# Performance work log

Hardware: AMD Instinct MI355X
Metric: run time of the kernel (lower is better)

Reference implementation:

```python
import jax, jax.numpy as jnp
import numpy as np

N_WIRES = 10
N_LAYERS = 4


def _cnot(state, c, t):
    # state: (2,)*N_WIRES per-sample state tensor; CNOT(control=c, target=t)
    s0 = jnp.take(state, 0, axis=c)
    s1 = jnp.take(state, 1, axis=c)
    tt = t if t < c else t - 1  # target axis index after removing control axis
    s1 = jnp.flip(s1, axis=tt)  # X on target where control == 1
    return jnp.stack([s0, s1], axis=c)


def _circuit(x, params):
    # x: (N_WIRES,) angles. RY(x_i) on |0> -> [cos(x_i/2), sin(x_i/2)] product state.
    q = jnp.stack([jnp.cos(x / 2), jnp.sin(x / 2)], axis=-1).astype(jnp.complex64)  # (n, 2)
    state = q[0]
    for i in range(1, N_WIRES):
        state = jnp.tensordot(state, q[i], axes=0)  # -> (2,)*N_WIRES
    half = jnp.array([-0.5, 0.5], dtype=jnp.float32)
    for layer in range(N_LAYERS):
        # RZ(params[layer, i]) on each wire: diagonal phase exp(-i*theta/2), exp(+i*theta/2)
        for i in range(N_WIRES):
            ph = jnp.exp(1j * (half * params[layer, i]))  # (2,) complex64
            shape = [1] * N_WIRES
            shape[i] = 2
            state = state * ph.reshape(shape)
        # CNOT ladder 0->1, 1->2, ..., (n-2)->(n-1), then (n-1)->0
        for i in range(N_WIRES - 1):
            state = _cnot(state, i, i + 1)
        state = _cnot(state, N_WIRES - 1, 0)
    return state.reshape(-1)  # (2**N_WIRES,)


def _states(X, params):
    return jax.vmap(lambda x: _circuit(x, params))(X)  # (B, 2**N_WIRES) complex64


def setup_inputs() -> dict:
    key = jax.random.key(0)
    k1, k2, k3 = jax.random.split(key, 3)
    two_pi = 2.0 * np.pi
    X = jax.random.uniform(k1, (4096, N_WIRES), jnp.float32, 0.0, two_pi)
    Y = jax.random.uniform(k2, (4096, N_WIRES), jnp.float32, 0.0, two_pi)
    params = jax.random.normal(k3, (N_LAYERS, N_WIRES), dtype=jnp.float32)
    return {"X": X, "Y": Y, "params": params}


def reference(X, Y, params):
    sX = _states(X, params)                 # (Nx, D) complex64
    sY = _states(Y, params)                 # (Ny, D) complex64
    M = sX @ sY.conj().T                    # (Nx, Ny) complex overlaps
    return M.real ** 2 + M.imag ** 2        # |<psi_x|psi_y>|^2
```

## Files before the change

### kernel.cpp

```cpp
#include <hip/hip_runtime.h>


#define NS 4096
#define NW 10
#define ROWS 32
#define CPT 2

__global__ __launch_bounds__(256) void qkm_fused(
    const float* __restrict__ X, const float* __restrict__ Y,
    float* __restrict__ out) {
    __shared__ float2 xcs[ROWS][NW];

    const int col  = (blockIdx.x * 256 + threadIdx.x) * CPT;
    const int row0 = blockIdx.y * ROWS;

    for (int t = threadIdx.x; t < ROWS * NW; t += 256) {
        int r = t / NW;
        int w = t - r * NW;
        float s, c;
        __sincosf(0.5f * X[(row0 + r) * NW + w], &s, &c);
        xcs[r][w] = make_float2(c, s);
    }

    float yc[NW][CPT], ys[NW][CPT];
#pragma unroll
    for (int j = 0; j < CPT; ++j) {
        const float* yp = Y + (size_t)(col + j) * NW;
#pragma unroll
        for (int w = 0; w < NW; ++w) {
            float s, c;
            __sincosf(0.5f * yp[w], &s, &c);
            yc[w][j] = c;
            ys[w][j] = s;
        }
    }

    __syncthreads();

#pragma unroll 4
    for (int r = 0; r < ROWS; ++r) {
        float p0 = 1.f, p1 = 1.f;
#pragma unroll
        for (int w = 0; w < NW; ++w) {
            const float2 x = xcs[r][w];
            p0 *= fmaf(x.y, ys[w][0], x.x * yc[w][0]);
            p1 *= fmaf(x.y, ys[w][1], x.x * yc[w][1]);
        }
        float2 o;
        o.x = p0 * p0;
        o.y = p1 * p1;
        *reinterpret_cast<float2*>(out + (size_t)(row0 + r) * NS + col) = o;
    }
}

extern "C" void kernel_launch(void* const* d_in, const int* in_sizes, int n_in,
                              void* d_out, int out_size, void* d_ws, size_t ws_size,
                              hipStream_t stream) {
    const float* X = (const float*)d_in[0];
    const float* Y = (const float*)d_in[1];
    float* out = (float*)d_out;

    dim3 grid(NS / (256 * CPT), NS / ROWS);
    qkm_fused<<<grid, 256, 0, stream>>>(X, Y, out);
}
```

Baseline: 89.36 us.

## Factor cos(x) into per-row product and use tan form with packed float2 math

Rewrites each factor cx*cy + sx*sy as cx*(cy + tan(x)*sy). The per-row product of cx is precomputed once per block, which removes one multiply per wire from the inner loop. The inner loop uses ext_vector float2 operations so the compiler can emit packed FMA instructions, and the row data is loaded with 128-bit shared-memory reads. Near-zero cosines are clamped to avoid division by zero, but large tangent values may hurt accuracy. The change also adds an extra block synchronisation.

After: 82.96 us. 1.08x faster.

```diff
diff --git a/kernel.cpp b/kernel.cpp
--- a/kernel.cpp
+++ b/kernel.cpp
@@ -6,10 +6,15 @@
 #define ROWS 32
 #define CPT 2
 
+typedef float v2f __attribute__((ext_vector_type(2)));
+
+static __device__ inline v2f splat2(float x) { v2f v; v.x = x; v.y = x; return v; }
+
 __global__ __launch_bounds__(256) void qkm_fused(
     const float* __restrict__ X, const float* __restrict__ Y,
     float* __restrict__ out) {
-    __shared__ float2 xcs[ROWS][NW];
+    __shared__ float xrow[ROWS][12];
+    __shared__ float cxa[ROWS][NW];
 
     const int col  = (blockIdx.x * 256 + threadIdx.x) * CPT;
     const int row0 = blockIdx.y * ROWS;
@@ -19,37 +24,44 @@
         int w = t - r * NW;
         float s, c;
         __sincosf(0.5f * X[(row0 + r) * NW + w], &s, &c);
-        xcs[r][w] = make_float2(c, s);
+        float cs = (fabsf(c) < 1e-30f) ? copysignf(1e-30f, c) : c;
+        xrow[r][w] = __fdividef(s, cs);
+        cxa[r][w]  = cs;
     }
 
-    float yc[NW][CPT], ys[NW][CPT];
+    v2f cy[NW], sy[NW];
 #pragma unroll
-    for (int j = 0; j < CPT; ++j) {
-        const float* yp = Y + (size_t)(col + j) * NW;
-#pragma unroll
-        for (int w = 0; w < NW; ++w) {
-            float s, c;
-            __sincosf(0.5f * yp[w], &s, &c);
-            yc[w][j] = c;
-            ys[w][j] = s;
-        }
+    for (int w = 0; w < NW; ++w) {
+        float s0, c0, s1, c1;
+        __sincosf(0.5f * Y[(size_t)col * NW + w], &s0, &c0);
+        __sincosf(0.5f * Y[(size_t)(col + 1) * NW + w], &s1, &c1);
+        v2f c; c.x = c0; c.y = c1;
+        v2f s; s.x = s0; s.y = s1;
+        cy[w] = c; sy[w] = s;
     }
 
+    __syncthreads();
+    if (threadIdx.x < ROWS) {
+        int r = threadIdx.x;
+        float p = cxa[r][0];
+#pragma unroll
+        for (int w = 1; w < NW; ++w) p *= cxa[r][w];
+        xrow[r][NW] = p;
+    }
     __syncthreads();
 
 #pragma unroll 4
     for (int r = 0; r < ROWS; ++r) {
-        float p0 = 1.f, p1 = 1.f;
+        float a[12];
+        *reinterpret_cast<float4*>(&a[0]) = *reinterpret_cast<const float4*>(&xrow[r][0]);
+        *reinterpret_cast<float4*>(&a[4]) = *reinterpret_cast<const float4*>(&xrow[r][4]);
+        *reinterpret_cast<float4*>(&a[8]) = *reinterpret_cast<const float4*>(&xrow[r][8]);
+        v2f p = splat2(a[NW]);
 #pragma unroll
-        for (int w = 0; w < NW; ++w) {
-            const float2 x = xcs[r][w];
-            p0 *= fmaf(x.y, ys[w][0], x.x * yc[w][0]);
-            p1 *= fmaf(x.y, ys[w][1], x.x * yc[w][1]);
-        }
-        float2 o;
-        o.x = p0 * p0;
-        o.y = p1 * p1;
-        *reinterpret_cast<float2*>(out + (size_t)(row0 + r) * NS + col) = o;
+        for (int w = 0; w < NW; ++w)
+            p = p * (cy[w] + splat2(a[w]) * sy[w]);
+        v2f o = p * p;
+        *reinterpret_cast<v2f*>(out + (size_t)(row0 + r) * NS + col) = o;
     }
 }
 
```
